# Kernel optimization log

Hardware: AMD Instinct MI355X
Metric: run time of the kernel (lower is better)

The kernel has to match this reference:

```python
import jax, jax.numpy as jnp
import numpy as np
from jax.ops import segment_sum, segment_max

LRELU = 0.01  # torch F.leaky_relu default negative_slope


def _seg_softmax(e, seg, n):
    # torch_geometric.utils.softmax: stable segment softmax with 1e-16 eps
    m = segment_max(e, seg, num_segments=n)
    ex = jnp.exp(e - m[seg])
    s = segment_sum(ex, seg, num_segments=n)
    return ex / (s[seg] + 1e-16)


def _gcn(x, ei, w):
    j, i = ei[0], ei[1]  # code unpacks (edge_index_j, edge_index_i)
    n = x.shape[0]
    deg = segment_sum(jnp.ones_like(x[:, 0])[i], i, num_segments=n)
    dis = jnp.where(deg > 0, deg ** -0.5, 0.0)
    norm = dis[j] * dis[i]
    agg = segment_sum(norm[:, None] * x[j], i, num_segments=n)  # out[i] += norm*x[j]
    return jax.nn.relu(agg) @ w


def _highway(x1, x2, w, b):
    gate = jax.nn.sigmoid(x1 @ w + b)
    return gate * x2 + (1.0 - gate) * x1


def _gat_r(x, ei, a_i, a_j):
    j, i = ei[0], ei[1]
    n = x.shape[0]
    si = x @ a_i  # [R]
    sj = x @ a_j
    e = si[i] + sj[j]
    alpha = _seg_softmax(jax.nn.leaky_relu(e, LRELU).astype(jnp.float32), j, n)  # grouped by j!
    return jax.nn.relu(segment_sum(alpha[:, None] * x[j], i, num_segments=n))


def _graphattention_wjq(x, ei, rel_all, rel_emb, ww1):
    i, j = ei[0], ei[1]  # this module unpacks (i, j)
    n = x.shape[0]
    ef = jax.nn.leaky_relu(x, LRELU)
    re = jax.nn.leaky_relu(rel_emb, LRELU)
    feat = jnp.concatenate([ef[i], re[rel_all], ef[j]], axis=1)  # [E, 700]
    att = _seg_softmax(feat @ ww1, i, n)
    return segment_sum(feat * att[:, None], i, num_segments=n)  # [N, 700]


def _gat(x, r, ei, rel, a_i, a_j, a_r):
    j, i = ei[0], ei[1]
    n = x.shape[0]
    e = (x @ a_i)[i] + (x @ a_j)[j] + (r @ a_r)[rel]
    alpha = _seg_softmax(jax.nn.leaky_relu(e, LRELU).astype(jnp.float32), i, n)
    return jax.nn.relu(segment_sum(alpha[:, None] * x[j], i, num_segments=n))


def setup_inputs() -> dict:
    key = jax.random.key(0)
    ks = jax.random.split(key, 24)
    N, E, R, ELG, EH, RH = 20000, 150000, 1000, 15000, 300, 100

    def edges(k, n_nodes, n_edges):
        k1, k2 = jax.random.split(k)
        src = jax.random.randint(k1, (n_edges,), 0, n_nodes)
        dst = jax.random.randint(k2, (n_edges,), 0, n_nodes)
        src = jnp.where(src == dst, (src + 1) % n_nodes, src)  # no self-loops
        ring = jnp.arange(n_nodes)  # guarantee in-degree >= 1 everywhere
        src = src.at[:n_nodes].set((ring + 1) % n_nodes)
        dst = dst.at[:n_nodes].set(ring)
        return jnp.stack([src, dst])  # row0 = j (source), row1 = i (target)

    rel = jax.random.randint(ks[3], (E,), 0, R).at[0].set(R - 1)  # branch -> rel_emb1
    p = lambda k, sh: (jax.random.normal(k, sh, jnp.float32) * 0.05)
    return {
        "x_e": jax.random.normal(ks[0], (N, EH), jnp.float32),
        "edge_index": edges(ks[1], N, E),
        "rel": rel,
        "edge_index_all": edges(ks[2], N, E),
        "rel_all": jax.random.randint(ks[4], (E,), 0, 2 * R),
        "line_graph_index_out": edges(ks[5], R, ELG),
        "line_graph_val_out": jax.random.normal(ks[6], (ELG,), jnp.float32),
        "line_graph_index_in": edges(ks[7], R, ELG),
        "line_graph_val_in": jax.random.normal(ks[8], (ELG,), jnp.float32),
        "gcn1_w": p(ks[9], (EH, EH)),
        "gcn2_w": p(ks[10], (EH, EH)),
        "hw1_w": p(ks[11], (EH, EH)),
        "hw1_b": jnp.zeros((EH,), jnp.float32),
        "hw2_w": p(ks[12], (EH, EH)),
        "hw2_b": jnp.zeros((EH,), jnp.float32),
        "ww1": p(ks[13], (2 * EH + RH,)),
        "gat_ai": p(ks[14], (2 * (2 * EH + RH) - 400 + 0,)) if False else p(ks[14], (1000,)),
        "gat_aj": p(ks[15], (1000,)),
        "gat_ar": p(ks[16], (RH,)),
        "gatr_ai": p(ks[17], (RH,)),
        "gatr_aj": p(ks[18], (RH,)),
        "rel_emb1": p(ks[19], (R, RH)),
        "rel_emb2": p(ks[20], (R, RH)),
    }


def reference(x_e, edge_index, rel, edge_index_all, rel_all,
              line_graph_index_out, line_graph_val_out,
              line_graph_index_in, line_graph_val_in,
              gcn1_w, gcn2_w, hw1_w, hw1_b, hw2_w, hw2_b, ww1,
              gat_ai, gat_aj, gat_ar, gatr_ai, gatr_aj, rel_emb1, rel_emb2):
    # RAGA.forward; inputs constructed so rel.max()+1 == rel_emb1.shape[0]
    # (branch taken) and edge_index_all has no self-loops (remove_self_loops no-op).
    x = _highway(x_e, _gcn(x_e, edge_index_all, gcn1_w), hw1_w, hw1_b)
    x = _highway(x, _gcn(x, edge_index_all, gcn2_w), hw2_w, hw2_b)
    rel_emb_out = _gat_r(rel_emb1, line_graph_index_out, gatr_ai, gatr_aj)
    rel_emb_in = _gat_r(rel_emb1, line_graph_index_in, gatr_ai, gatr_aj)
    rel_emb = jnp.concatenate([rel_emb_out, rel_emb_in], axis=0)  # [2R, 100]
    x_wjq = jnp.concatenate(
        [x, _graphattention_wjq(x, edge_index_all, rel_all, rel_emb, ww1)], axis=1)  # [N, 1000]
    out = jnp.concatenate(
        [x_wjq, _gat(x_wjq, rel_emb, edge_index_all, rel_all, gat_ai, gat_aj, gat_ar)], axis=1)
    return out  # [N, 2000]
```

## Files before the change

### kernel.cpp

```cpp
#include <hip/hip_runtime.h>
#include <math.h>

#define LSL 0.01f

typedef _Float16 half8 __attribute__((ext_vector_type(8)));
typedef _Float16 half4 __attribute__((ext_vector_type(4)));
typedef float floatx4 __attribute__((ext_vector_type(4)));

static __device__ __forceinline__ float lrelu_f(float x){ return x > 0.f ? x : LSL * x; }
static __device__ __forceinline__ void atomAddF(float* p, float v){ unsafeAtomicAdd(p, v); }

__global__ __launch_bounds__(256)
void k_setup(const int* __restrict__ dstA, const int* __restrict__ srcA,
             int* __restrict__ degD, int* __restrict__ degS, int E,
             const float* __restrict__ W0, const float* __restrict__ W1,
             const float* __restrict__ W2, const float* __restrict__ W3,
             _Float16* __restrict__ BfAll,
             const float* __restrict__ x_e, _Float16* __restrict__ xh0,
             float* __restrict__ sxi, float* __restrict__ sxj, int N,
             const float* __restrict__ relEmb1, const float* __restrict__ gatr_ai,
             const float* __restrict__ gatr_aj, float* __restrict__ sR_i,
             float* __restrict__ sR_j, int R, int B0, int B1, int B2){
  int b = blockIdx.x, t = threadIdx.x;
  if (b < B0){
    int e = b * 256 + t;
    if (e < E){ atomicAdd(degD + dstA[e], 1); atomicAdd(degS + srcA[e], 1); }
  } else if (b < B0 + B1){
    int idx = (b - B0) * 256 + t;
    if (idx >= 4*12800) return;
    int wsel = idx / 12800;
    int rem2 = idx % 12800;
    const float* W = (wsel == 0) ? W0 : (wsel == 1) ? W1 : (wsel == 2) ? W2 : W3;
    int lane = rem2 & 63;
    int rem = rem2 >> 6;
    int nf = rem & 3; rem >>= 2;
    int nt = rem % 5;
    int ks = rem / 5;
    int n = nt*64 + nf*16 + (lane & 15);
    int kb = ks*32 + (lane >> 4) * 8;
    _Float16* o = BfAll + (size_t)wsel * 102400 + (size_t)rem2 * 8;
    #pragma unroll
    for (int e = 0; e < 8; e++){
      int k = kb + e;
      float v = (k < 300 && n < 300) ? W[(size_t)k * 300 + n] : 0.f;
      o[e] = (_Float16)v;
    }
  } else if (b < B0 + B1 + B2){
    int i = b - B0 - B1;
    _Float16* o = xh0 + (size_t)i * 320;
    if (i < N){
      const float* r = x_e + (size_t)i * 300;
      o[t] = (_Float16)r[t];
      if (t < 44) o[t + 256] = (_Float16)r[t + 256];
      else if (t < 64) o[t + 256] = (_Float16)0.f;
      if (t == 0) sxi[i] = 0.f;
      if (t == 1) sxj[i] = 0.f;
    } else {
      o[t] = (_Float16)0.f;
      if (t < 64) o[t + 256] = (_Float16)0.f;
    }
  } else {
    int v = (b - B0 - B1 - B2) * 256 + t;
    if (v >= R) return;
    const float* row = relEmb1 + (size_t)v * 100;
    float a = 0.f, c = 0.f;
    for (int k = 0; k < 100; k++){
      float f = row[k];
      a += f * gatr_ai[k];
      c += f * gatr_aj[k];
    }
    sR_i[v] = a;
    sR_j[v] = c;
  }
}

__global__ __launch_bounds__(1024)
void k_scan2(const int* __restrict__ cntD, int* __restrict__ offD,
             const int* __restrict__ cntS, int* __restrict__ offS, int n){
  const int* cnt = blockIdx.x ? cntS : cntD;
  int* off = blockIdx.x ? offS : offD;
  int t = threadIdx.x, lane = t & 63, wid = t >> 6;
  int len = (n + 1023) >> 10;
  int lo = t * len, hi = min(lo + len, n);
  int s = 0;
  for (int k = lo; k < hi; k++) s += cnt[k];
  int ws = s;
  #pragma unroll
  for (int o = 1; o < 64; o <<= 1){
    int u = __shfl_up(ws, o);
    if (lane >= o) ws += u;
  }
  __shared__ int wtot[16];
  if (lane == 63) wtot[wid] = ws;
  __syncthreads();
  int wpre = 0;
  #pragma unroll
  for (int k2 = 0; k2 < 16; k2++) wpre += (k2 < wid) ? wtot[k2] : 0;
  int run = wpre + ws - s;
  for (int k = lo; k < hi; k++){ off[k] = run; run += cnt[k]; }
  if (t == 0){
    int tot = 0;
    #pragma unroll
    for (int k2 = 0; k2 < 16; k2++) tot += wtot[k2];
    off[n] = tot;
  }
}

__global__ void k_fill_inv(const int* __restrict__ dstA, const int* __restrict__ srcA,
                           const int* __restrict__ offD, const int* __restrict__ offS,
                           int* __restrict__ curD, int* __restrict__ curS,
                           int* __restrict__ permD, int* __restrict__ permS,
                           const int* __restrict__ degD, float* __restrict__ dis,
                           int E, int N, int FB){
  int b = blockIdx.x, t = threadIdx.x;
  if (b < FB){
    int e = b * 256 + t;
    if (e >= E) return;
    int i = dstA[e];
    permD[offD[i] + atomicAdd(curD + i, 1)] = e;
    int j = srcA[e];
    permS[offS[j] + atomicAdd(curS + j, 1)] = e;
  } else {
    int v = (b - FB) * 256 + t;
    if (v < N){ int d = degD[v]; dis[v] = d > 0 ? rsqrtf((float)d) : 0.f; }
  }
}

__global__ __launch_bounds__(256)
void k_gcn_gather(const int* __restrict__ off, const int* __restrict__ perm,
                  const int* __restrict__ src, const _Float16* __restrict__ x,
                  const float* __restrict__ dis, _Float16* __restrict__ agg, int N){
  int i = (int)(((long)blockIdx.x * blockDim.x + threadIdx.x) >> 6);
  int lane = threadIdx.x & 63;
  if (i >= N) return;
  int p0 = off[i], p1 = off[i+1];
  float di = dis[i];
  float acc[8] = {0.f,0.f,0.f,0.f,0.f,0.f,0.f,0.f};
  for (int base = p0; base < p1; base += 64){
    int m = min(64, p1 - base);
    int jj = 0; float wl = 0.f;
    if (base + lane < p1){
      int e = perm[base + lane];
      jj = src[e];
      wl = di * dis[jj];
    }
    int q = 0;
    for (; q + 1 < m; q += 2){
      int j0 = __shfl(jj, q),   j1 = __shfl(jj, q+1);
      float w0 = __shfl(wl, q), w1 = __shfl(wl, q+1);
      if (lane < 40){
        half8 v0 = *(const half8*)(x + (size_t)j0 * 320 + 8*lane);
        half8 v1 = *(const half8*)(x + (size_t)j1 * 320 + 8*lane);
        #pragma unroll
        for (int k = 0; k < 8; k++) acc[k] += w0 * (float)v0[k] + w1 * (float)v1[k];
      }
    }
    if (q < m){
      int j0 = __shfl(jj, q);
      float w0 = __shfl(wl, q);
      if (lane < 40){
        half8 v0 = *(const half8*)(x + (size_t)j0 * 320 + 8*lane);
        #pragma unroll
        for (int k = 0; k < 8; k++) acc[k] += w0 * (float)v0[k];
      }
    }
  }
  if (lane < 40){
    half8 o;
    #pragma unroll
    for (int k = 0; k < 8; k++) o[k] = (_Float16)fmaxf(acc[k], 0.f);
    *(half8*)(agg + (size_t)i * 320 + 8*lane) = o;
  }
}

__global__ __launch_bounds__(256)
void k_dual_mfma(const _Float16* __restrict__ A1, const _Float16* __restrict__ Xh,
                 const _Float16* __restrict__ Bf1, const _Float16* __restrict__ Bf2,
                 const float* __restrict__ bias, float* __restrict__ Of32, long ldo,
                 _Float16* __restrict__ Oh, long ldm, int M,
                 const float* __restrict__ ww, float* __restrict__ sxi,
                 float* __restrict__ sxj){
  int nb = gridDim.x;
  int q = nb >> 3, r = nb & 7;
  int xcd = blockIdx.x & 7, kk0 = blockIdx.x >> 3;
  int pseudo = (xcd < r ? xcd * (q + 1) : r * (q + 1) + (xcd - r) * q) + kk0;
  int nt = pseudo % 5;
  int panel = pseudo / 5;

  int tid = threadIdx.x;
  int w = tid >> 6, lane = tid & 63;
  int l15 = lane & 15, lg = lane >> 4;
  int rowBase = panel * 64 + w * 16;
  int colBase = nt * 64;

  floatx4 acc1[4], acc2[4];
  #pragma unroll
  for (int b = 0; b < 4; b++){
    acc1[b] = (floatx4){0.f,0.f,0.f,0.f};
    acc2[b] = (floatx4){0.f,0.f,0.f,0.f};
  }

  int row0 = rowBase + l15;
  const _Float16* a1p0 = A1 + (size_t)row0 * 320;
  const _Float16* a2p0 = Xh + (size_t)row0 * 320;

  for (int ks = 0; ks < 10; ks++){
    int kA = ks*32 + lg*8;
    half8 a1f0 = *(const half8*)(a1p0 + kA);
    half8 a2f0 = *(const half8*)(a2p0 + kA);
    const half8* b1p = (const half8*)Bf1 + ((size_t)(ks*5 + nt) * 4 * 64 + lane);
    const half8* b2p = (const half8*)Bf2 + ((size_t)(ks*5 + nt) * 4 * 64 + lane);
    #pragma unroll
    for (int nf = 0; nf < 4; nf++){
      half8 b1 = b1p[nf*64];
      half8 b2 = b2p[nf*64];
      acc1[nf] = __builtin_amdgcn_mfma_f32_16x16x32_f16(a1f0, b1, acc1[nf], 0,0,0);
      acc2[nf] = __builtin_amdgcn_mfma_f32_16x16x32_f16(a2f0, b2, acc2[nf], 0,0,0);
    }
  }

  bool doSX = (sxi != nullptr);
  float dA[4] = {0.f,0.f,0.f,0.f}, dB[4] = {0.f,0.f,0.f,0.f};
  #pragma unroll
  for (int nf = 0; nf < 4; nf++){
    int gn = colBase + nf*16 + l15;
    int gnc = min(gn, 299);
    float bv = bias[gnc];
    float wA = doSX ? ww[gnc] : 0.f;
    float wB = doSX ? ww[400 + gnc] : 0.f;
    #pragma unroll
    for (int r2 = 0; r2 < 4; r2++){
      int gm = rowBase + lg*4 + r2;
      int gmc = min(gm, M-1);
      float xv = (float)Xh[(size_t)gmc * 320 + gnc];
      float g = 1.f / (1.f + expf(-(acc2[nf][r2] + bv)));
      float val = g * acc1[nf][r2] + (1.f - g) * xv;
      if (gm < M && gn < 300){
        if (Of32) Of32[(size_t)gm * ldo + gn] = val;
        if (Oh)   Oh[(size_t)gm * ldm + gn] = (_Float16)val;
        float f = lrelu_f(val);
        dA[r2] += f * wA;
        dB[r2] += f * wB;
      }
    }
  }
  if (doSX){
    #pragma unroll
    for (int r2 = 0; r2 < 4; r2++){
      float a = dA[r2], b = dB[r2];
      #pragma unroll
      for (int o = 1; o < 16; o <<= 1){
        a += __shfl_xor(a, o);
        b += __shfl_xor(b, o);
      }
      int gm = rowBase + lg*4 + r2;
      if (l15 == 0 && gm < M){
        atomAddF(sxi + gm, a);
        atomAddF(sxj + gm, b);
      }
    }
  }
}

__global__ __launch_bounds__(256)
void k_wjq_gather(const int* __restrict__ off, const int* __restrict__ perm,
                  const int* __restrict__ dstA, const int* __restrict__ relI,
                  const float* __restrict__ sxi, const float* __restrict__ sxj,
                  const float* __restrict__ aRel, const _Float16* __restrict__ relEmbH,
                  const float* __restrict__ gat_ai, const float* __restrict__ gat_aj,
                  float* __restrict__ out, _Float16* __restrict__ xh2,
                  float* __restrict__ gxi, float* __restrict__ gxj,
                  float* __restrict__ sAl, int N){
  int i = (int)(((long)blockIdx.x * blockDim.x + threadIdx.x) >> 6);
  int lane = threadIdx.x & 63;
  if (i >= N) return;
  int p0 = off[i], p1 = off[i+1];
  int deg = p1 - p0;
  float si = sxi[i];
  float accx[8] = {0.f,0.f,0.f,0.f,0.f,0.f,0.f,0.f};
  float accr[4] = {0.f,0.f,0.f,0.f};
  float sumA;

  if (deg <= 64){
    int jj = 0, rr = 0; float l = -3.4e38f;
    if (lane < deg){
      int e = perm[p0 + lane];
      jj = dstA[e]; rr = relI[e];
      l = si + sxj[jj] + aRel[rr];
    }
    float lm = l;
    #pragma unroll
    for (int o = 32; o > 0; o >>= 1) lm = fmaxf(lm, __shfl_xor(lm, o));
    float exl = (lane < deg) ? expf(l - lm) : 0.f;
    float ls = exl;
    #pragma unroll
    for (int o = 32; o > 0; o >>= 1) ls += __shfl_xor(ls, o);
    float inv = 1.f / (ls + 1e-16f);
    sumA = ls * inv;
    float wgt = exl * inv;
    int qe = 0;
    for (; qe + 1 < deg; qe += 2){
      int j0 = __shfl(jj, qe),  j1 = __shfl(jj, qe+1);
      int r0 = __shfl(rr, qe),  r1 = __shfl(rr, qe+1);
      float a0 = __shfl(wgt, qe), a1 = __shfl(wgt, qe+1);
      if (lane < 38){
        half8 v0 = *(const half8*)(xh2 + (size_t)j0 * 1024 + 8*lane);
        half8 v1 = *(const half8*)(xh2 + (size_t)j1 * 1024 + 8*lane);
        #pragma unroll
        for (int k = 0; k < 8; k++)
          accx[k] += a0 * lrelu_f((float)v0[k]) + a1 * lrelu_f((float)v1[k]);
      } else if (lane < 63){
        half4 v0 = *(const half4*)(relEmbH + (size_t)r0 * 100 + 4*(lane - 38));
        half4 v1 = *(const half4*)(relEmbH + (size_t)r1 * 100 + 4*(lane - 38));
        #pragma unroll
        for (int k = 0; k < 4; k++)
          accr[k] += a0 * (float)v0[k] + a1 * (float)v1[k];
      }
    }
    if (qe < deg){
      int j0 = __shfl(jj, qe);
      int r0 = __shfl(rr, qe);
      float a0 = __shfl(wgt, qe);
      if (lane < 38){
        half8 v0 = *(const half8*)(xh2 + (size_t)j0 * 1024 + 8*lane);
        #pragma unroll
        for (int k = 0; k < 8; k++) accx[k] += a0 * lrelu_f((float)v0[k]);
      } else if (lane < 63){
        half4 v0 = *(const half4*)(relEmbH + (size_t)r0 * 100 + 4*(lane - 38));
        #pragma unroll
        for (int k = 0; k < 4; k++) accr[k] += a0 * (float)v0[k];
      }
    }
  } else {
    float lm = -3.4e38f;
    for (int p = p0 + lane; p < p1; p += 64){
      int e = perm[p];
      lm = fmaxf(lm, si + sxj[dstA[e]] + aRel[relI[e]]);
    }
    #pragma unroll
    for (int o = 32; o > 0; o >>= 1) lm = fmaxf(lm, __shfl_xor(lm, o));
    float ls = 0.f;
    for (int p = p0 + lane; p < p1; p += 64){
      int e = perm[p];
      ls += expf(si + sxj[dstA[e]] + aRel[relI[e]] - lm);
    }
    #pragma unroll
    for (int o = 32; o > 0; o >>= 1) ls += __shfl_xor(ls, o);
    float inv = 1.f / (ls + 1e-16f);
    sumA = ls * inv;
    for (int base = p0; base < p1; base += 64){
      int m = min(64, p1 - base);
      int jj = 0, rr = 0; float all = 0.f;
      if (base + lane < p1){
        int e = perm[base + lane];
        jj = dstA[e]; rr = relI[e];
        all = expf(si + sxj[jj] + aRel[rr] - lm) * inv;
      }
      for (int qe = 0; qe < m; qe++){
        int j = __shfl(jj, qe);
        int r = __shfl(rr, qe);
        float al = __shfl(all, qe);
        if (lane < 38){
          half8 v = *(const half8*)(xh2 + (size_t)j * 1024 + 8*lane);
          #pragma unroll
          for (int k = 0; k < 8; k++) accx[k] += al * lrelu_f((float)v[k]);
        } else if (lane < 63){
          half4 v = *(const half4*)(relEmbH + (size_t)r * 100 + 4*(lane - 38));
          #pragma unroll
          for (int k = 0; k < 4; k++) accr[k] += al * (float)v[k];
        }
      }
    }
  }

  float* oi = out + (size_t)i * 2000;
  _Float16* hi = xh2 + (size_t)i * 1024;
  float dA = 0.f, dB = 0.f;
  if (lane < 38){
    #pragma unroll
    for (int k = 0; k < 8; k++){
      int c = 8*lane + k;
      if (c < 300){
        oi[700 + c] = accx[k]; hi[700 + c] = (_Float16)accx[k];
        dA += accx[k] * gat_ai[700 + c];
        dB += accx[k] * gat_aj[700 + c];
      }
    }
    half8 v = *(const half8*)(hi + 8*lane);
    #pragma unroll
    for (int k = 0; k < 8; k++){
      int c = 8*lane + k;
      if (c < 300){
        float x2v = (float)v[k];
        float h = lrelu_f(x2v) * sumA;
        oi[300 + c] = h;
        dA += x2v * gat_ai[c] + h * gat_ai[300 + c];
        dB += x2v * gat_aj[c] + h * gat_aj[300 + c];
      }
    }
  } else if (lane < 63){
    #pragma unroll
    for (int k = 0; k < 4; k++){
      int c = 4*(lane - 38) + k;
      oi[600 + c] = accr[k]; hi[600 + c] = (_Float16)accr[k];
      dA += accr[k] * gat_ai[600 + c];
      dB += accr[k] * gat_aj[600 + c];
    }
  }
  #pragma unroll
  for (int o = 32; o > 0; o >>= 1){
    dA += __shfl_xor(dA, o);
    dB += __shfl_xor(dB, o);
  }
  if (lane == 0){ gxi[i] = dA; gxj[i] = dB; sAl[i] = sumA; }
}

__global__ __launch_bounds__(256)
void k_gat_gather(const int* __restrict__ off, const int* __restrict__ perm,
                  const int* __restrict__ srcA, const int* __restrict__ relI,
                  const float* __restrict__ gxi, const float* __restrict__ gxj,
                  const float* __restrict__ srr, const float* __restrict__ sAl,
                  const _Float16* __restrict__ xh2, float* __restrict__ out, int N){
  long gw = ((long)blockIdx.x * blockDim.x + threadIdx.x) >> 6;
  int lane = threadIdx.x & 63;
  int i = (int)(gw / 3), part = (int)(gw % 3);
  if (i >= N) return;
  int p0 = off[i], p1 = off[i+1];
  int deg = p1 - p0;
  float gi = gxi[i];
  int cbase = (part == 0) ? 0 : (400 + part * 200);
  int c0 = cbase + 8*lane;
  bool act = (part == 0) ? (lane < 38) : (lane < 25);
  float acc_a[8] = {0.f,0.f,0.f,0.f,0.f,0.f,0.f,0.f};
  float acc_b[8] = {0.f,0.f,0.f,0.f,0.f,0.f,0.f,0.f};

  if (deg <= 64){
    int jj = 0; float l = -3.4e38f, saj = 0.f;
    if (lane < deg){
      int e = perm[p0 + lane];
      jj = srcA[e];
      l = lrelu_f(gi + gxj[jj] + srr[relI[e]]);
      if (part == 0) saj = sAl[jj];
    }
    float lm = l;
    #pragma unroll
    for (int o = 32; o > 0; o >>= 1) lm = fmaxf(lm, __shfl_xor(lm, o));
    float exl = (lane < deg) ? expf(l - lm) : 0.f;
    float ls = exl;
    #pragma unroll
    for (int o = 32; o > 0; o >>= 1) ls += __shfl_xor(ls, o);
    float wgt = exl / (ls + 1e-16f);
    if (part == 0){
      int qe = 0;
      for (; qe + 1 < deg; qe += 2){
        int j0 = __shfl(jj, qe),    j1 = __shfl(jj, qe+1);
        float a0 = __shfl(wgt, qe), a1 = __shfl(wgt, qe+1);
        float s0 = __shfl(saj, qe) * a0, s1 = __shfl(saj, qe+1) * a1;
        if (act){
          half8 v0 = *(const half8*)(xh2 + (size_t)j0 * 1024 + 8*lane);
          half8 v1 = *(const half8*)(xh2 + (size_t)j1 * 1024 + 8*lane);
          #pragma unroll
          for (int k = 0; k < 8; k++){
            float x0 = (float)v0[k], x1 = (float)v1[k];
            acc_a[k] += a0 * x0 + a1 * x1;
            acc_b[k] += s0 * lrelu_f(x0) + s1 * lrelu_f(x1);
          }
        }
      }
      if (qe < deg){
        int j0 = __shfl(jj, qe);
        float a0 = __shfl(wgt, qe);
        float s0 = __shfl(saj, qe) * a0;
        if (act){
          half8 v0 = *(const half8*)(xh2 + (size_t)j0 * 1024 + 8*lane);
          #pragma unroll
          for (int k = 0; k < 8; k++){
            float x0 = (float)v0[k];
            acc_a[k] += a0 * x0;
            acc_b[k] += s0 * lrelu_f(x0);
          }
        }
      }
    } else {
      int qe = 0;
      for (; qe + 1 < deg; qe += 2){
        int j0 = __shfl(jj, qe),    j1 = __shfl(jj, qe+1);
        float a0 = __shfl(wgt, qe), a1 = __shfl(wgt, qe+1);
        if (act){
          half8 v0 = *(const half8*)(xh2 + (size_t)j0 * 1024 + c0);
          half8 v1 = *(const half8*)(xh2 + (size_t)j1 * 1024 + c0);
          #pragma unroll
          for (int k = 0; k < 8; k++) acc_a[k] += a0 * (float)v0[k] + a1 * (float)v1[k];
        }
      }
      if (qe < deg){
        int j0 = __shfl(jj, qe);
        float a0 = __shfl(wgt, qe);
        if (act){
          half8 v0 = *(const half8*)(xh2 + (size_t)j0 * 1024 + c0);
          #pragma unroll
          for (int k = 0; k < 8; k++) acc_a[k] += a0 * (float)v0[k];
        }
      }
    }
  } else {
    float lm = -3.4e38f;
    for (int p = p0 + lane; p < p1; p += 64){
      int e = perm[p];
      lm = fmaxf(lm, lrelu_f(gi + gxj[srcA[e]] + srr[relI[e]]));
    }
    #pragma unroll
    for (int o = 32; o > 0; o >>= 1) lm = fmaxf(lm, __shfl_xor(lm, o));
    float ls = 0.f;
    for (int p = p0 + lane; p < p1; p += 64){
      int e = perm[p];
      ls += expf(lrelu_f(gi + gxj[srcA[e]] + srr[relI[e]]) - lm);
    }
    #pragma unroll
    for (int o = 32; o > 0; o >>= 1) ls += __shfl_xor(ls, o);
    float inv = 1.f / (ls + 1e-16f);
    for (int base = p0; base < p1; base += 64){
      int m = min(64, p1 - base);
      int jj = 0; float all = 0.f, saj = 0.f;
      if (base + lane < p1){
        int e = perm[base + lane];
        jj = srcA[e];
        all = expf(lrelu_f(gi + gxj[jj] + srr[relI[e]]) - lm) * inv;
        if (part == 0) saj = sAl[jj];
      }
      for (int qe = 0; qe < m; qe++){
        int j = __shfl(jj, qe);
        float al = __shfl(all, qe);
        if (part == 0){
          float sa = __shfl(saj, qe) * al;
          if (act){
            half8 v = *(const half8*)(xh2 + (size_t)j * 1024 + 8*lane);
            #pragma unroll
            for (int k = 0; k < 8; k++){
              float x0 = (float)v[k];
              acc_a[k] += al * x0;
              acc_b[k] += sa * lrelu_f(x0);
            }
          }
        } else {
          if (act){
            half8 v = *(const half8*)(xh2 + (size_t)j * 1024 + c0);
            #pragma unroll
            for (int k = 0; k < 8; k++) acc_a[k] += al * (float)v[k];
          }
        }
      }
    }
  }

  float* ob = out + (size_t)i * 2000 + 1000;
  if (part == 0){
    if (lane < 37){
      floatx4 s0, s1, t0, t1;
      #pragma unroll
      for (int k = 0; k < 4; k++){
        s0[k] = fmaxf(acc_a[k], 0.f);   s1[k] = fmaxf(acc_a[4+k], 0.f);
        t0[k] = fmaxf(acc_b[k], 0.f);   t1[k] = fmaxf(acc_b[4+k], 0.f);
      }
      *(floatx4*)(ob + 8*lane) = s0;
      *(floatx4*)(ob + 8*lane + 4) = s1;
      *(floatx4*)(ob + 300 + 8*lane) = t0;
      *(floatx4*)(ob + 300 + 8*lane + 4) = t1;
    } else if (lane == 37){
      #pragma unroll
      for (int k = 0; k < 4; k++){
        ob[296 + k] = fmaxf(acc_a[k], 0.f);
        ob[596 + k] = fmaxf(acc_b[k], 0.f);
      }
    }
  } else {
    if (lane < 25){
      floatx4 s0, s1;
      #pragma unroll
      for (int k = 0; k < 4; k++){ s0[k] = fmaxf(acc_a[k], 0.f); s1[k] = fmaxf(acc_a[4+k], 0.f); }
      *(floatx4*)(ob + c0) = s0;
      *(floatx4*)(ob + c0 + 4) = s1;
    }
  }
}

__global__ void k_relu_dots(float* __restrict__ relEmb, _Float16* __restrict__ relEmbH,
                            const float* __restrict__ wA, const float* __restrict__ wB,
                            float* __restrict__ aRel, float* __restrict__ srr, int n){
  int v = blockIdx.x * blockDim.x + threadIdx.x;
  if (v >= n) return;
  float* row = relEmb + (size_t)v * 100;
  _Float16* rowH = relEmbH + (size_t)v * 100;
  float a = 0.f, b = 0.f;
  for (int c = 0; c < 100; c++){
    float f = fmaxf(row[c], 0.f);
    row[c] = f;
    rowH[c] = (_Float16)f;
    a += f * wA[c];
    b += f * wB[c];
  }
  aRel[v] = a;
  srr[v] = b;
}

__global__ void k_lg_le(const int* __restrict__ lgOut, const int* __restrict__ lgIn,
                        int ELG, int R, const float* __restrict__ sR_i,
                        const float* __restrict__ sR_j,
                        float* __restrict__ elog, float* __restrict__ sumR){
  int e = blockIdx.x * blockDim.x + threadIdx.x;
  if (e >= 2*ELG) return;
  int g = e >= ELG;
  int el = e - g*ELG;
  const int* lg = g ? lgIn : lgOut;
  int j = lg[el], i = lg[el + ELG];
  float ex = expf(lrelu_f(sR_j[j] + sR_i[i]));
  elog[e] = ex;
  atomAddF(sumR + g*R + j, ex);
}

__global__ void k_lg_scatter(const int* __restrict__ lgOut, const int* __restrict__ lgIn,
                             int ELG, int R, const float* __restrict__ ex,
                             const float* __restrict__ sumR,
                             const float* __restrict__ relEmb1, float* __restrict__ relEmb){
  int e = blockIdx.x;
  int g = e >= ELG;
  int el = e - g*ELG;
  const int* lg = g ? lgIn : lgOut;
  int j = lg[el], i = lg[el + ELG];
  float alpha = ex[e] / (sumR[g*R + j] + 1e-16f);
  const float* xj = relEmb1 + (size_t)j * 100;
  float* oi = relEmb + (size_t)(g*R + i) * 100;
  for (int c = threadIdx.x; c < 100; c += blockDim.x)
    atomAddF(oi + c, alpha * xj[c]);
}

extern "C" void kernel_launch(void* const* d_in, const int* in_sizes, int n_in,
                              void* d_out, int out_size, void* d_ws, size_t ws_size,
                              hipStream_t stream){
  const float* x_e     = (const float*)d_in[0];
  const int*   eiA     = (const int*)  d_in[3];
  const int*   relAll  = (const int*)  d_in[4];
  const int*   lgOut   = (const int*)  d_in[5];
  const int*   lgIn    = (const int*)  d_in[7];
  const float* gcn1_w  = (const float*)d_in[9];
  const float* gcn2_w  = (const float*)d_in[10];
  const float* hw1_w   = (const float*)d_in[11];
  const float* hw1_b   = (const float*)d_in[12];
  const float* hw2_w   = (const float*)d_in[13];
  const float* hw2_b   = (const float*)d_in[14];
  const float* ww1     = (const float*)d_in[15];
  const float* gat_ai  = (const float*)d_in[16];
  const float* gat_aj  = (const float*)d_in[17];
  const float* gat_ar  = (const float*)d_in[18];
  const float* gatr_ai = (const float*)d_in[19];
  const float* gatr_aj = (const float*)d_in[20];
  const float* relEmb1 = (const float*)d_in[21];

  const int EH = 300, RH = 100;
  const int N   = in_sizes[0] / EH;
  const int E   = in_sizes[3] / 2;
  const int ELG = in_sizes[5] / 2;
  const int R   = in_sizes[21] / RH;
  const int Mtiles = (N + 127) / 128;
  const int Mpad = Mtiles * 128;

  char* base = (char*)d_ws;
  _Float16* xh0   = (_Float16*)base;  base += (size_t)Mpad * 320 * 2;
  _Float16* xhA   = (_Float16*)base;  base += (size_t)Mpad * 320 * 2;
  _Float16* A1f16 = (_Float16*)base;  base += (size_t)Mpad * 320 * 2;
  _Float16* xh2   = (_Float16*)base;  base += (size_t)N * 1024 * 2;
  _Float16* BfAll = (_Float16*)base;  base += (size_t)4 * 102400 * 2;
  _Float16* relEmbH = (_Float16*)base; base += (size_t)2 * R * RH * 2;
  float* w = (float*)base;
  float* dis    = w; w += N;
  float* relEmb = w; w += (size_t)2 * R * RH;
  float* sumR   = w; w += 2 * R;
  float* sxi    = w; w += N;
  float* sxj    = w; w += N;
  float* gxi    = w; w += N;
  float* gxj    = w; w += N;
  float* sAl    = w; w += N;
  float* sR_i   = w; w += R;
  float* sR_j   = w; w += R;
  float* aRel   = w; w += 2 * R;
  float* srr    = w; w += 2 * R;
  float* eE     = w; w += E;
  int* degD   = (int*)w; w += N;
  int* degS   = (int*)w; w += N;
  int* curD   = (int*)w; w += N;
  int* curS   = (int*)w; w += N;
  int* offD   = (int*)w; w += N + 1;
  int* offS   = (int*)w; w += N + 1;
  int* permD  = (int*)w; w += E;
  int* permS  = (int*)w; w += E;

  _Float16* Bf_g1 = BfAll;
  _Float16* Bf_h1 = BfAll + 102400;
  _Float16* Bf_g2 = BfAll + 2 * 102400;
  _Float16* Bf_h2 = BfAll + 3 * 102400;

  float* out = (float*)d_out;
  const int* srcA = eiA;
  const int* dstA = eiA + E;

  auto cdiv = [](int a, int b){ return (a + b - 1) / b; };

  hipMemsetAsync(degD, 0, (size_t)4 * N * 4, stream);
  int B0 = cdiv(E,256), B1 = 200, B2 = Mpad, B3 = cdiv(R,256);
  k_setup<<<B0+B1+B2+B3,256,0,stream>>>(dstA, srcA, degD, degS, E,
                                        gcn1_w, hw1_w, gcn2_w, hw2_w, BfAll,
                                        x_e, xh0, sxi, sxj, N,
                                        relEmb1, gatr_ai, gatr_aj, sR_i, sR_j, R,
                                        B0, B1, B2);
  k_scan2<<<2,1024,0,stream>>>(degD, offD, degS, offS, N);
  int FB = cdiv(E,256);
  k_fill_inv<<<FB + cdiv(N,256),256,0,stream>>>(dstA, srcA, offD, offS, curD, curS,
                                                permD, permS, degD, dis, E, N, FB);

  int NB = 5 * (Mpad / 64);
  int GW = cdiv(N, 4);

  k_gcn_gather<<<GW,256,0,stream>>>(offD, permD, srcA, xh0, dis, A1f16, N);
  k_dual_mfma<<<NB,256,0,stream>>>(A1f16, xh0, Bf_g1, Bf_h1, hw1_b,
                                   nullptr, 0, xhA, 320, N, nullptr, nullptr, nullptr);

  k_gcn_gather<<<GW,256,0,stream>>>(offD, permD, srcA, xhA, dis, A1f16, N);
  k_dual_mfma<<<NB,256,0,stream>>>(A1f16, xhA, Bf_g2, Bf_h2, hw2_b,
                                   out, 2000, xh2, 1024, N, ww1, sxi, sxj);

  hipMemsetAsync(relEmb, 0, ((size_t)2*R*RH + 2*R) * 4, stream);
  k_lg_le<<<cdiv(2*ELG,256),256,0,stream>>>(lgOut, lgIn, ELG, R, sR_i, sR_j, eE, sumR);
  k_lg_scatter<<<2*ELG,128,0,stream>>>(lgOut, lgIn, ELG, R, eE, sumR, relEmb1, relEmb);

  k_relu_dots<<<cdiv(2*R,256),256,0,stream>>>(relEmb, relEmbH, ww1 + EH, gat_ar, aRel, srr, 2*R);

  k_wjq_gather<<<GW,256,0,stream>>>(offS, permS, dstA, relAll, sxi, sxj, aRel, relEmbH,
                                    gat_ai, gat_aj, out, xh2, gxi, gxj, sAl, N);

  k_gat_gather<<<cdiv(3*N,4),256,0,stream>>>(offD, permD, srcA, relAll, gxi, gxj, srr,
                                             sAl, xh2, out, N);
}
```

Before: 373.6 us.

## Fold line-graph relation attention kernels into GCN gather and MFMA launches

The three small line-graph kernels (edge logits, scatter, relu+dots) are removed and run as extra blocks appended to the existing gcn_gather and dual_mfma launches, so independent relation-embedding work overlaps with the entity pipeline and three launches disappear. The memset of relEmb moves to the start. The gcn gather also restricts active lanes from 40 to 38, which skips the padding columns beyond 300 but leaves those output columns unwritten. The added blocks inflate grids and register pressure of the shared kernels.

```diff
diff --git a/kernel.cpp b/kernel.cpp
--- a/kernel.cpp
+++ b/kernel.cpp
@@ -129,7 +129,43 @@
 __global__ __launch_bounds__(256)
 void k_gcn_gather(const int* __restrict__ off, const int* __restrict__ perm,
                   const int* __restrict__ src, const _Float16* __restrict__ x,
-                  const float* __restrict__ dis, _Float16* __restrict__ agg, int N){
+                  const float* __restrict__ dis, _Float16* __restrict__ agg, int N,
+                  int GWB, int mode,
+                  const int* __restrict__ lgOut, const int* __restrict__ lgIn,
+                  int ELG, int R, const float* __restrict__ sR_i,
+                  const float* __restrict__ sR_j, float* __restrict__ eE,
+                  float* __restrict__ sumR,
+                  float* __restrict__ relEmb, _Float16* __restrict__ relEmbH,
+                  const float* __restrict__ wA, const float* __restrict__ wB,
+                  float* __restrict__ aRel, float* __restrict__ srr){
+  if (blockIdx.x >= GWB){
+    int idx = (blockIdx.x - GWB) * 256 + threadIdx.x;
+    if (mode == 1){
+      if (idx >= 2*ELG) return;
+      int g = idx >= ELG;
+      int el = idx - g*ELG;
+      const int* lg = g ? lgIn : lgOut;
+      int j = lg[el], i2 = lg[el + ELG];
+      float ex = expf(lrelu_f(sR_j[j] + sR_i[i2]));
+      eE[idx] = ex;
+      atomAddF(sumR + g*R + j, ex);
+    } else {
+      if (idx >= 2*R) return;
+      float* row = relEmb + (size_t)idx * 100;
+      _Float16* rowH = relEmbH + (size_t)idx * 100;
+      float a = 0.f, b2 = 0.f;
+      for (int c = 0; c < 100; c++){
+        float f = fmaxf(row[c], 0.f);
+        row[c] = f;
+        rowH[c] = (_Float16)f;
+        a += f * wA[c];
+        b2 += f * wB[c];
+      }
+      aRel[idx] = a;
+      srr[idx] = b2;
+    }
+    return;
+  }
   int i = (int)(((long)blockIdx.x * blockDim.x + threadIdx.x) >> 6);
   int lane = threadIdx.x & 63;
   if (i >= N) return;
@@ -148,7 +184,7 @@
     for (; q + 1 < m; q += 2){
       int j0 = __shfl(jj, q),   j1 = __shfl(jj, q+1);
       float w0 = __shfl(wl, q), w1 = __shfl(wl, q+1);
-      if (lane < 40){
+      if (lane < 38){
         half8 v0 = *(const half8*)(x + (size_t)j0 * 320 + 8*lane);
         half8 v1 = *(const half8*)(x + (size_t)j1 * 320 + 8*lane);
         #pragma unroll
@@ -158,14 +194,14 @@
     if (q < m){
       int j0 = __shfl(jj, q);
       float w0 = __shfl(wl, q);
-      if (lane < 40){
+      if (lane < 38){
         half8 v0 = *(const half8*)(x + (size_t)j0 * 320 + 8*lane);
         #pragma unroll
         for (int k = 0; k < 8; k++) acc[k] += w0 * (float)v0[k];
       }
     }
   }
-  if (lane < 40){
+  if (lane < 38){
     half8 o;
     #pragma unroll
     for (int k = 0; k < 8; k++) o[k] = (_Float16)fmaxf(acc[k], 0.f);
@@ -179,8 +215,27 @@
                  const float* __restrict__ bias, float* __restrict__ Of32, long ldo,
                  _Float16* __restrict__ Oh, long ldm, int M,
                  const float* __restrict__ ww, float* __restrict__ sxi,
-                 float* __restrict__ sxj){
-  int nb = gridDim.x;
+                 float* __restrict__ sxj, int NBm,
+                 const int* __restrict__ lgOut, const int* __restrict__ lgIn,
+                 int ELG, int R, const float* __restrict__ eE,
+                 const float* __restrict__ sumR, const float* __restrict__ relEmb1,
+                 float* __restrict__ relEmbO){
+  if (blockIdx.x >= NBm){
+    int t = threadIdx.x;
+    int e = (blockIdx.x - NBm) * 2 + (t >> 7);
+    if (e >= 2*ELG) return;
+    int g = e >= ELG;
+    int el = e - g*ELG;
+    const int* lg = g ? lgIn : lgOut;
+    int j = lg[el], i2 = lg[el + ELG];
+    float alpha = eE[e] / (sumR[g*R + j] + 1e-16f);
+    int tt = t & 127;
+    if (tt < 100)
+      atomAddF(relEmbO + (size_t)(g*R + i2) * 100 + tt,
+               alpha * relEmb1[(size_t)j * 100 + tt]);
+    return;
+  }
+  int nb = NBm;
   int q = nb >> 3, r = nb & 7;
   int xcd = blockIdx.x & 7, kk0 = blockIdx.x >> 3;
   int pseudo = (xcd < r ? xcd * (q + 1) : r * (q + 1) + (xcd - r) * q) + kk0;
@@ -189,7 +244,7 @@
 
   int tid = threadIdx.x;
   int w = tid >> 6, lane = tid & 63;
-  int l15 = lane & 15, lg = lane >> 4;
+  int l15 = lane & 15, lg2 = lane >> 4;
   int rowBase = panel * 64 + w * 16;
   int colBase = nt * 64;
 
@@ -205,7 +260,7 @@
   const _Float16* a2p0 = Xh + (size_t)row0 * 320;
 
   for (int ks = 0; ks < 10; ks++){
-    int kA = ks*32 + lg*8;
+    int kA = ks*32 + lg2*8;
     half8 a1f0 = *(const half8*)(a1p0 + kA);
     half8 a2f0 = *(const half8*)(a2p0 + kA);
     const half8* b1p = (const half8*)Bf1 + ((size_t)(ks*5 + nt) * 4 * 64 + lane);
@@ -230,7 +285,7 @@
     float wB = doSX ? ww[400 + gnc] : 0.f;
     #pragma unroll
     for (int r2 = 0; r2 < 4; r2++){
-      int gm = rowBase + lg*4 + r2;
+      int gm = rowBase + lg2*4 + r2;
       int gmc = min(gm, M-1);
       float xv = (float)Xh[(size_t)gmc * 320 + gnc];
       float g = 1.f / (1.f + expf(-(acc2[nf][r2] + bv)));
@@ -253,7 +308,7 @@
         a += __shfl_xor(a, o);
         b += __shfl_xor(b, o);
       }
-      int gm = rowBase + lg*4 + r2;
+      int gm = rowBase + lg2*4 + r2;
       if (l15 == 0 && gm < M){
         atomAddF(sxi + gm, a);
         atomAddF(sxj + gm, b);
@@ -582,56 +637,6 @@
       *(floatx4*)(ob + c0 + 4) = s1;
     }
   }
-}
-
-__global__ void k_relu_dots(float* __restrict__ relEmb, _Float16* __restrict__ relEmbH,
-                            const float* __restrict__ wA, const float* __restrict__ wB,
-                            float* __restrict__ aRel, float* __restrict__ srr, int n){
-  int v = blockIdx.x * blockDim.x + threadIdx.x;
-  if (v >= n) return;
-  float* row = relEmb + (size_t)v * 100;
-  _Float16* rowH = relEmbH + (size_t)v * 100;
-  float a = 0.f, b = 0.f;
-  for (int c = 0; c < 100; c++){
-    float f = fmaxf(row[c], 0.f);
-    row[c] = f;
-    rowH[c] = (_Float16)f;
-    a += f * wA[c];
-    b += f * wB[c];
-  }
-  aRel[v] = a;
-  srr[v] = b;
-}
-
-__global__ void k_lg_le(const int* __restrict__ lgOut, const int* __restrict__ lgIn,
-                        int ELG, int R, const float* __restrict__ sR_i,
-                        const float* __restrict__ sR_j,
-                        float* __restrict__ elog, float* __restrict__ sumR){
-  int e = blockIdx.x * blockDim.x + threadIdx.x;
-  if (e >= 2*ELG) return;
-  int g = e >= ELG;
-  int el = e - g*ELG;
-  const int* lg = g ? lgIn : lgOut;
-  int j = lg[el], i = lg[el + ELG];
-  float ex = expf(lrelu_f(sR_j[j] + sR_i[i]));
-  elog[e] = ex;
-  atomAddF(sumR + g*R + j, ex);
-}
-
-__global__ void k_lg_scatter(const int* __restrict__ lgOut, const int* __restrict__ lgIn,
-                             int ELG, int R, const float* __restrict__ ex,
-                             const float* __restrict__ sumR,
-                             const float* __restrict__ relEmb1, float* __restrict__ relEmb){
-  int e = blockIdx.x;
-  int g = e >= ELG;
-  int el = e - g*ELG;
-  const int* lg = g ? lgIn : lgOut;
-  int j = lg[el], i = lg[el + ELG];
-  float alpha = ex[e] / (sumR[g*R + j] + 1e-16f);
-  const float* xj = relEmb1 + (size_t)j * 100;
-  float* oi = relEmb + (size_t)(g*R + i) * 100;
-  for (int c = threadIdx.x; c < 100; c += blockDim.x)
-    atomAddF(oi + c, alpha * xj[c]);
 }
 
 extern "C" void kernel_launch(void* const* d_in, const int* in_sizes, int n_in,
@@ -706,6 +711,7 @@
   auto cdiv = [](int a, int b){ return (a + b - 1) / b; };
 
   hipMemsetAsync(degD, 0, (size_t)4 * N * 4, stream);
+  hipMemsetAsync(relEmb, 0, ((size_t)2*R*RH + 2*R) * 4, stream);
   int B0 = cdiv(E,256), B1 = 200, B2 = Mpad, B3 = cdiv(R,256);
   k_setup<<<B0+B1+B2+B3,256,0,stream>>>(dstA, srcA, degD, degS, E,
                                         gcn1_w, hw1_w, gcn2_w, hw2_w, BfAll,
@@ -719,20 +725,23 @@
 
   int NB = 5 * (Mpad / 64);
   int GW = cdiv(N, 4);
-
-  k_gcn_gather<<<GW,256,0,stream>>>(offD, permD, srcA, xh0, dis, A1f16, N);
-  k_dual_mfma<<<NB,256,0,stream>>>(A1f16, xh0, Bf_g1, Bf_h1, hw1_b,
-                                   nullptr, 0, xhA, 320, N, nullptr, nullptr, nullptr);
-
-  k_gcn_gather<<<GW,256,0,stream>>>(offD, permD, srcA, xhA, dis, A1f16, N);
+  int EXT1 = cdiv(2*ELG, 256);
+  int EXT2 = cdiv(2*R, 256);
+
+  k_gcn_gather<<<GW+EXT1,256,0,stream>>>(offD, permD, srcA, xh0, dis, A1f16, N,
+                                         GW, 1, lgOut, lgIn, ELG, R, sR_i, sR_j, eE, sumR,
+                                         nullptr, nullptr, nullptr, nullptr, nullptr, nullptr);
+  k_dual_mfma<<<NB+ELG,256,0,stream>>>(A1f16, xh0, Bf_g1, Bf_h1, hw1_b,
+                                       nullptr, 0, xhA, 320, N, nullptr, nullptr, nullptr,
+                                       NB, lgOut, lgIn, ELG, R, eE, sumR, relEmb1, relEmb);
+  k_gcn_gather<<<GW+EXT2,256,0,stream>>>(offD, permD, srcA, xhA, dis, A1f16, N,
+                                         GW, 2, nullptr, nullptr, ELG, R, nullptr, nullptr,
+                                         nullptr, nullptr,
+                                         relEmb, relEmbH, ww1 + EH, gat_ar, aRel, srr);
   k_dual_mfma<<<NB,256,0,stream>>>(A1f16, xhA, Bf_g2, Bf_h2, hw2_b,
-                                   out, 2000, xh2, 1024, N, ww1, sxi, sxj);
-
-  hipMemsetAsync(relEmb, 0, ((size_t)2*R*RH + 2*R) * 4, stream);
-  k_lg_le<<<cdiv(2*ELG,256),256,0,stream>>>(lgOut, lgIn, ELG, R, sR_i, sR_j, eE, sumR);
-  k_lg_scatter<<<2*ELG,128,0,stream>>>(lgOut, lgIn, ELG, R, eE, sumR, relEmb1, relEmb);
-
-  k_relu_dots<<<cdiv(2*R,256),256,0,stream>>>(relEmb, relEmbH, ww1 + EH, gat_ar, aRel, srr, 2*R);
+                                   out, 2000, xh2, 1024, N, ww1, sxi, sxj,
+                                   NB, nullptr, nullptr, ELG, R, nullptr, nullptr,
+                                   nullptr, nullptr);
 
   k_wjq_gather<<<GW,256,0,stream>>>(offS, permS, dstA, relAll, sxi, sxj, aRel, relEmbH,
                                     gat_ai, gat_aj, out, xh2, gxi, gxj, sAl, N);
```

Result: faster. 361.9 us (-3.1%).
